# Performance work log

Measured on AMD Instinct MI355X. Metric: run time of the kernel, lower is better.

## Reference

```python
import jax, jax.numpy as jnp
import numpy as np

INPUT_DIM = 1024
HIDDEN_DIM = 1024

def setup_inputs() -> dict:
    key = jax.random.key(0)
    ks = jax.random.split(key, 9)
    s_in = 1.0 / np.sqrt(INPUT_DIM)
    s_h = 1.0 / np.sqrt(HIDDEN_DIM)
    x = jax.random.normal(ks[0], (4, 2048, INPUT_DIM), dtype=jnp.float32)
    Wq = jax.random.uniform(ks[1], (INPUT_DIM, HIDDEN_DIM), jnp.float32, -s_in, s_in)
    bq = jax.random.uniform(ks[2], (HIDDEN_DIM,), jnp.float32, -s_in, s_in)
    Wk = jax.random.uniform(ks[3], (INPUT_DIM, HIDDEN_DIM), jnp.float32, -s_in, s_in)
    bk = jax.random.uniform(ks[4], (HIDDEN_DIM,), jnp.float32, -s_in, s_in)
    Wv = jax.random.uniform(ks[5], (INPUT_DIM, HIDDEN_DIM), jnp.float32, -s_in, s_in)
    bv = jax.random.uniform(ks[6], (HIDDEN_DIM,), jnp.float32, -s_in, s_in)
    Wo = jax.random.uniform(ks[7], (HIDDEN_DIM, INPUT_DIM), jnp.float32, -s_h, s_h)
    bo = jax.random.uniform(ks[8], (INPUT_DIM,), jnp.float32, -s_h, s_h)
    return {"x": x, "Wq": Wq, "bq": bq, "Wk": Wk, "bk": bk, "Wv": Wv, "bv": bv, "Wo": Wo, "bo": bo}

def reference(x, Wq, bq, Wk, bk, Wv, bv, Wo, bo):
    # x: [B, S, D_in]; scale uses x.shape[-1] (faithful to source, which divides by sqrt(input_dim))
    scale = 1.0 / jnp.sqrt(jnp.asarray(x.shape[-1], dtype=x.dtype))
    Q = jnp.einsum('bsd,dh->bsh', x, Wq) + bq
    K = jnp.einsum('bsd,dh->bsh', x, Wk) + bk
    V = jnp.einsum('bsd,dh->bsh', x, Wv) + bv
    scores = jnp.einsum('bqh,bkh->bqk', Q, K) * scale  # [B, S, S]
    attn = jax.nn.softmax(scores, axis=-1)
    ctx = jnp.einsum('bqk,bkh->bqh', attn, V)
    return jnp.einsum('bsh,hd->bsd', ctx, Wo) + bo
```

## Files before the change

### kernel.cpp

```cpp
#include <hip/hip_runtime.h>

typedef __attribute__((ext_vector_type(8))) short bf16x8;
typedef __attribute__((ext_vector_type(4))) float f32x4;
typedef __attribute__((ext_vector_type(4))) unsigned short us4;

#define AS1 __attribute__((address_space(1)))
#define AS3 __attribute__((address_space(3)))

__device__ __forceinline__ unsigned short f2bf(float f) {
  unsigned u = __float_as_uint(f);
  u += 0x7fff + ((u >> 16) & 1);
  return (unsigned short)(u >> 16);
}

__device__ __forceinline__ void gload_lds16(const void* g, void* l) {
  __builtin_amdgcn_global_load_lds((const AS1 unsigned int*)g,
                                   (AS3 unsigned int*)l, 16, 0, 0);
}

#define MFMA16(a, b, c) __builtin_amdgcn_mfma_f32_16x16x32_bf16(a, b, c, 0, 0, 0)

template <typename OutT, bool BIAS, int MODE>
__global__ __launch_bounds__(512, 2) void gemm8p(
    const unsigned short* __restrict__ A,
    const unsigned short* __restrict__ Bt,
    OutT* __restrict__ C,
    unsigned short* __restrict__ Vt,
    const float* __restrict__ bias,
    int Kd, int lda, int ldb, int ldc,
    long sA, long sB, long sC,
    float scale) {
  constexpr int BOFF = 256 * 64;
  __shared__ unsigned short lds[2][512 * 64];

  const int bz = blockIdx.z;
  A  += (size_t)bz * sA + (size_t)blockIdx.x * 256 * lda;
  Bt += (size_t)bz * sB + (size_t)blockIdx.y * 256 * ldb;

  const int tid  = threadIdx.x;
  const int wave = tid >> 6;
  const int lane = tid & 63;
  const int wm   = wave >> 2;
  const int wn   = wave & 3;
  const int l15  = lane & 15;
  const int hi   = lane >> 4;
  const int sr  = (wave << 3) + (lane >> 3);
  const int sc8 = lane & 7;
  const int co0 = ((hi    ) ^ (lane & 7)) << 3;
  const int co1 = ((hi + 4) ^ (lane & 7)) << 3;
  const int rA0 = wm * 128 + l15;
  const int rB0 = wn * 32 + l15;

  auto stA = [&](int b, int k0, int r0) {
    const unsigned short* g =
        A + (size_t)(r0 + sr) * lda + (k0 + ((sc8 ^ (sr & 7)) << 3));
    gload_lds16(g, &lds[b][(r0 + (wave << 3)) * 64]);
  };
  auto stB = [&](int b, int k0, int r0) {
    const int lr = r0 + sr;
    const int gr = ((lr >> 5) & 3) * 64 + ((lr >> 7) << 5) + (lr & 31);
    const unsigned short* g =
        Bt + (size_t)gr * ldb + (k0 + ((sc8 ^ (lr & 7)) << 3));
    gload_lds16(g, &lds[b][BOFF + (r0 + (wave << 3)) * 64]);
  };

  f32x4 acc[8][4] = {};
  bf16x8 af[4][2], b0f[2][2], b1f[2][2];

  stA(0, 0, 0);   stA(0, 0, 128);
  stB(0, 0, 0);   stB(0, 0, 64);
  stB(0, 0, 128); stB(0, 0, 192);
  stA(0, 0, 64);  stA(0, 0, 192);
  asm volatile("s_waitcnt vmcnt(4)" ::: "memory");
  __builtin_amdgcn_s_barrier();

  const int NT = Kd >> 6;
  for (int t = 0; t < NT; ++t) {
    const int buf = t & 1;
    const int nb  = buf ^ 1;
    const int nk0 = (t + 1) << 6;
    const bool st = (t + 1) < NT;
    const unsigned short* Lr = &lds[buf][0];

#pragma unroll
    for (int mt = 0; mt < 4; ++mt) {
      af[mt][0] = *(const bf16x8*)&Lr[(rA0 + mt * 16) * 64 + co0];
      af[mt][1] = *(const bf16x8*)&Lr[(rA0 + mt * 16) * 64 + co1];
    }
#pragma unroll
    for (int n = 0; n < 2; ++n) {
      b0f[n][0] = *(const bf16x8*)&Lr[BOFF + (rB0 + n * 16) * 64 + co0];
      b0f[n][1] = *(const bf16x8*)&Lr[BOFF + (rB0 + n * 16) * 64 + co1];
    }
    if (st) { stA(nb, nk0, 0); stA(nb, nk0, 128); }
    __builtin_amdgcn_s_barrier();
    __builtin_amdgcn_s_setprio(1);
#pragma unroll
    for (int mt = 0; mt < 4; ++mt)
#pragma unroll
      for (int n = 0; n < 2; ++n) {
        acc[mt][n] = MFMA16(af[mt][0], b0f[n][0], acc[mt][n]);
        acc[mt][n] = MFMA16(af[mt][1], b0f[n][1], acc[mt][n]);
      }
    __builtin_amdgcn_s_setprio(0);
    asm volatile("s_waitcnt vmcnt(4)" ::: "memory");
    __builtin_amdgcn_s_barrier();

#pragma unroll
    for (int n = 0; n < 2; ++n) {
      b1f[n][0] = *(const bf16x8*)&Lr[BOFF + (128 + rB0 + n * 16) * 64 + co0];
      b1f[n][1] = *(const bf16x8*)&Lr[BOFF + (128 + rB0 + n * 16) * 64 + co1];
    }
    if (st) { stB(nb, nk0, 0); stB(nb, nk0, 64); }
    __builtin_amdgcn_s_barrier();
    __builtin_amdgcn_s_setprio(1);
#pragma unroll
    for (int mt = 0; mt < 4; ++mt)
#pragma unroll
      for (int n = 0; n < 2; ++n) {
        acc[mt][2 + n] = MFMA16(af[mt][0], b1f[n][0], acc[mt][2 + n]);
        acc[mt][2 + n] = MFMA16(af[mt][1], b1f[n][1], acc[mt][2 + n]);
      }
    __builtin_amdgcn_s_setprio(0);
    asm volatile("s_waitcnt vmcnt(4)" ::: "memory");
    __builtin_amdgcn_s_barrier();

#pragma unroll
    for (int mt = 0; mt < 4; ++mt) {
      af[mt][0] = *(const bf16x8*)&Lr[(64 + rA0 + mt * 16) * 64 + co0];
      af[mt][1] = *(const bf16x8*)&Lr[(64 + rA0 + mt * 16) * 64 + co1];
    }
    if (st) { stB(nb, nk0, 128); stB(nb, nk0, 192); }
    __builtin_amdgcn_s_barrier();
    __builtin_amdgcn_s_setprio(1);
#pragma unroll
    for (int mt = 0; mt < 4; ++mt)
#pragma unroll
      for (int n = 0; n < 2; ++n) {
        acc[4 + mt][2 + n] = MFMA16(af[mt][0], b1f[n][0], acc[4 + mt][2 + n]);
        acc[4 + mt][2 + n] = MFMA16(af[mt][1], b1f[n][1], acc[4 + mt][2 + n]);
      }
    __builtin_amdgcn_s_setprio(0);
    __builtin_amdgcn_s_barrier();

    if (st) { stA(nb, nk0, 64); stA(nb, nk0, 192); }
    __builtin_amdgcn_s_barrier();
    __builtin_amdgcn_s_setprio(1);
#pragma unroll
    for (int mt = 0; mt < 4; ++mt)
#pragma unroll
      for (int n = 0; n < 2; ++n) {
        acc[4 + mt][n] = MFMA16(af[mt][0], b0f[n][0], acc[4 + mt][n]);
        acc[4 + mt][n] = MFMA16(af[mt][1], b0f[n][1], acc[4 + mt][n]);
      }
    __builtin_amdgcn_s_setprio(0);
    asm volatile("s_waitcnt vmcnt(4)" ::: "memory");
    __builtin_amdgcn_s_barrier();
  }

  const int hi4  = hi << 2;
  const int row0 = blockIdx.x * 256 + wm * 128;
  const int col0 = blockIdx.y * 256 + wn * 64;

  if constexpr (MODE == 1) {
#pragma unroll
    for (int nt = 0; nt < 4; ++nt) {
      const int gcol  = col0 + nt * 16;
      const int piece = gcol >> 10;
      const float bv  = BIAS ? bias[gcol + l15] : 0.0f;
      if (piece < 2) {
        OutT* dst = C + (size_t)piece * sC;
        const int col = (gcol & 1023) + l15;
#pragma unroll
        for (int mt = 0; mt < 8; ++mt)
#pragma unroll
          for (int r = 0; r < 4; ++r) {
            const int row = row0 + mt * 16 + hi4 + r;
            dst[(size_t)row * ldc + col] = (OutT)f2bf(acc[mt][nt][r] * scale + bv);
          }
      } else {
        const int d = (gcol & 1023) + l15;
        const int b = blockIdx.x >> 3;
        const int sb = (blockIdx.x & 7) * 256 + wm * 128 + hi4;
#pragma unroll
        for (int mt = 0; mt < 8; ++mt) {
          us4 pk;
          pk.x = f2bf(acc[mt][nt][0] * scale + bv);
          pk.y = f2bf(acc[mt][nt][1] * scale + bv);
          pk.z = f2bf(acc[mt][nt][2] * scale + bv);
          pk.w = f2bf(acc[mt][nt][3] * scale + bv);
          *(us4*)&Vt[((size_t)b << 21) + (size_t)d * 2048 + sb + mt * 16] = pk;
        }
      }
    }
  } else {
    C += (size_t)bz * sC;
#pragma unroll
    for (int nt = 0; nt < 4; ++nt) {
      const int col = col0 + nt * 16 + l15;
      const float bv = BIAS ? bias[col] : 0.0f;
#pragma unroll
      for (int mt = 0; mt < 8; ++mt)
#pragma unroll
        for (int r = 0; r < 4; ++r) {
          const int row = row0 + mt * 16 + hi4 + r;
          const float v = acc[mt][nt][r] * scale + bv;
          if constexpr (sizeof(OutT) == 4)
            C[(size_t)row * ldc + col] = v;
          else
            C[(size_t)row * ldc + col] = (OutT)f2bf(v);
        }
    }
  }
}

__global__ void cvt_x(const float* __restrict__ in, unsigned short* __restrict__ out, int n4) {
  const int i = blockIdx.x * blockDim.x + threadIdx.x;
  if (i < n4) {
    const float4 v = ((const float4*)in)[i];
    uint2 o;
    o.x = (unsigned)f2bf(v.x) | ((unsigned)f2bf(v.y) << 16);
    o.y = (unsigned)f2bf(v.z) | ((unsigned)f2bf(v.w) << 16);
    ((uint2*)out)[i] = o;
  }
}

__global__ void cvtT_w4(const float* __restrict__ Wq, const float* __restrict__ Wk,
                        const float* __restrict__ Wv, const float* __restrict__ Wo,
                        unsigned short* __restrict__ Wqkvb, unsigned short* __restrict__ Wob) {
  __shared__ unsigned short tile[64][65];
  const int z = blockIdx.z;
  const float* in = (z == 0) ? Wq : (z == 1) ? Wk : (z == 2) ? Wv : Wo;
  unsigned short* out = (z == 3) ? Wob : Wqkvb + (size_t)z * 1024 * 1024;
  const int r0 = blockIdx.y * 64, c0 = blockIdx.x * 64;
  for (int i = threadIdx.y; i < 64; i += 4)
    tile[i][threadIdx.x] = f2bf(in[(size_t)(r0 + i) * 1024 + c0 + threadIdx.x]);
  __syncthreads();
  for (int i = threadIdx.y; i < 64; i += 4)
    out[(size_t)(c0 + i) * 1024 + r0 + threadIdx.x] = tile[threadIdx.x][i];
}

__global__ void concat_bias(const float* __restrict__ bq, const float* __restrict__ bk,
                            const float* __restrict__ bv, float* __restrict__ dst) {
  const int z = blockIdx.x;
  const float* src = (z == 0) ? bq : (z == 1) ? bk : bv;
  const int i = threadIdx.x;
  ((float4*)(dst + z * 1024))[i] = ((const float4*)src)[i];
}

__global__ __launch_bounds__(256) void softmax_bf16(unsigned short* __restrict__ scores) {
  unsigned short* p = scores + (size_t)blockIdx.x * 2048;
  const int t = threadIdx.x;
  uint4 raw = ((const uint4*)p)[t];
  float v[8];
  v[0] = __uint_as_float(raw.x << 16); v[1] = __uint_as_float(raw.x & 0xffff0000u);
  v[2] = __uint_as_float(raw.y << 16); v[3] = __uint_as_float(raw.y & 0xffff0000u);
  v[4] = __uint_as_float(raw.z << 16); v[5] = __uint_as_float(raw.z & 0xffff0000u);
  v[6] = __uint_as_float(raw.w << 16); v[7] = __uint_as_float(raw.w & 0xffff0000u);

  float m = v[0];
#pragma unroll
  for (int i = 1; i < 8; ++i) m = fmaxf(m, v[i]);
#pragma unroll
  for (int off = 32; off; off >>= 1) m = fmaxf(m, __shfl_xor(m, off, 64));

  __shared__ float red[4];
  __shared__ float bcast[2];
  const int wave = t >> 6, lane = t & 63;
  if (lane == 0) red[wave] = m;
  __syncthreads();
  if (t == 0) bcast[0] = fmaxf(fmaxf(red[0], red[1]), fmaxf(red[2], red[3]));
  __syncthreads();
  m = bcast[0];

  float s = 0.f;
#pragma unroll
  for (int i = 0; i < 8; ++i) { v[i] = __expf(v[i] - m); s += v[i]; }
#pragma unroll
  for (int off = 32; off; off >>= 1) s += __shfl_xor(s, off, 64);
  if (lane == 0) red[wave] = s;
  __syncthreads();
  if (t == 0) bcast[1] = red[0] + red[1] + red[2] + red[3];
  __syncthreads();
  const float inv = 1.0f / bcast[1];

  uint4 ov;
  ov.x = (unsigned)f2bf(v[0] * inv) | ((unsigned)f2bf(v[1] * inv) << 16);
  ov.y = (unsigned)f2bf(v[2] * inv) | ((unsigned)f2bf(v[3] * inv) << 16);
  ov.z = (unsigned)f2bf(v[4] * inv) | ((unsigned)f2bf(v[5] * inv) << 16);
  ov.w = (unsigned)f2bf(v[6] * inv) | ((unsigned)f2bf(v[7] * inv) << 16);
  ((uint4*)p)[t] = ov;
}

extern "C" void kernel_launch(void* const* d_in, const int* in_sizes, int n_in,
                              void* d_out, int out_size, void* d_ws, size_t ws_size,
                              hipStream_t stream) {
  const float* x  = (const float*)d_in[0];
  const float* Wq = (const float*)d_in[1];
  const float* bq = (const float*)d_in[2];
  const float* Wk = (const float*)d_in[3];
  const float* bk = (const float*)d_in[4];
  const float* Wv = (const float*)d_in[5];
  const float* bv = (const float*)d_in[6];
  const float* Wo = (const float*)d_in[7];
  const float* bo = (const float*)d_in[8];
  float* out = (float*)d_out;

  char* ws = (char*)d_ws;
  size_t off = 0;
  auto alloc = [&](size_t bytes) { char* p = ws + off; off += (bytes + 255) & ~255UL; return p; };
  unsigned short* xb    = (unsigned short*)alloc(8192UL * 1024 * 2);
  unsigned short* Wqkvb = (unsigned short*)alloc(3072UL * 1024 * 2);
  unsigned short* Wob   = (unsigned short*)alloc(1024UL * 1024 * 2);
  float*          bqkv  = (float*)alloc(3072UL * 4);
  unsigned short* Qb    = (unsigned short*)alloc(8192UL * 1024 * 2);
  unsigned short* Kb    = (unsigned short*)alloc(8192UL * 1024 * 2);
  unsigned short* Vtb   = (unsigned short*)alloc(4UL * 1024 * 2048 * 2);
  unsigned short* attn  = (unsigned short*)alloc(8192UL * 2048 * 2);
  unsigned short* ctxb  = (unsigned short*)alloc(8192UL * 1024 * 2);

  const dim3 blk(512);

  cvt_x<<<2097152 / 256, 256, 0, stream>>>(x, xb, 2097152);
  cvtT_w4<<<dim3(16, 16, 4), dim3(64, 4), 0, stream>>>(Wq, Wk, Wv, Wo, Wqkvb, Wob);
  concat_bias<<<3, 256, 0, stream>>>(bq, bk, bv, bqkv);

  gemm8p<unsigned short, true, 1><<<dim3(32, 12, 1), blk, 0, stream>>>(
      xb, Wqkvb, Qb, Vtb, bqkv, 1024, 1024, 1024, 1024, 0, 0, 8192L * 1024, 1.0f);

  gemm8p<unsigned short, false, 0><<<dim3(8, 8, 4), blk, 0, stream>>>(
      Qb, Kb, attn, nullptr, nullptr, 1024, 1024, 1024, 2048,
      2048L * 1024, 2048L * 1024, 2048L * 2048, 0.03125f);

  softmax_bf16<<<8192, 256, 0, stream>>>(attn);

  gemm8p<unsigned short, false, 0><<<dim3(8, 4, 4), blk, 0, stream>>>(
      attn, Vtb, ctxb, nullptr, nullptr, 2048, 2048, 2048, 1024,
      2048L * 2048, 1024L * 2048, 2048L * 1024, 1.0f);

  gemm8p<float, true, 0><<<dim3(32, 4, 1), blk, 0, stream>>>(
      ctxb, Wob, out, nullptr, bo, 1024, 1024, 1024, 1024, 0, 0, 0, 1.0f);
}
```

Before: 328.4 us.

## Issue next-tile global loads earlier and reorder epilogue stores by row

Moves all of the next K-tile's global-to-LDS loads into the first two phases of the main loop, so prefetch is issued earlier and the waitcnts are relaxed, letting memory latency overlap more MFMA work. The vmcnt wait on the last iteration becomes vmcnt(0). The epilogue is also restructured to hoist bias loads and to write all four column tiles for each row together, which gives better write locality. Issuing loads in a burst may raise contention, and the changed wait counts must still match the number of outstanding loads.

New measurement: 323.4 us. About the same (-1.5%).

```diff
diff --git a/kernel.cpp b/kernel.cpp
--- a/kernel.cpp
+++ b/kernel.cpp
@@ -92,7 +92,7 @@
       b0f[n][0] = *(const bf16x8*)&Lr[BOFF + (rB0 + n * 16) * 64 + co0];
       b0f[n][1] = *(const bf16x8*)&Lr[BOFF + (rB0 + n * 16) * 64 + co1];
     }
-    if (st) { stA(nb, nk0, 0); stA(nb, nk0, 128); }
+    if (st) { stA(nb, nk0, 0); stA(nb, nk0, 128); stB(nb, nk0, 0); stB(nb, nk0, 64); }
     __builtin_amdgcn_s_barrier();
     __builtin_amdgcn_s_setprio(1);
 #pragma unroll
@@ -103,7 +103,8 @@
         acc[mt][n] = MFMA16(af[mt][1], b0f[n][1], acc[mt][n]);
       }
     __builtin_amdgcn_s_setprio(0);
-    asm volatile("s_waitcnt vmcnt(4)" ::: "memory");
+    if (st) asm volatile("s_waitcnt vmcnt(4)" ::: "memory");
+    else    asm volatile("s_waitcnt vmcnt(0)" ::: "memory");
     __builtin_amdgcn_s_barrier();
 
 #pragma unroll
@@ -111,7 +112,7 @@
       b1f[n][0] = *(const bf16x8*)&Lr[BOFF + (128 + rB0 + n * 16) * 64 + co0];
       b1f[n][1] = *(const bf16x8*)&Lr[BOFF + (128 + rB0 + n * 16) * 64 + co1];
     }
-    if (st) { stB(nb, nk0, 0); stB(nb, nk0, 64); }
+    if (st) { stB(nb, nk0, 128); stB(nb, nk0, 192); stA(nb, nk0, 64); stA(nb, nk0, 192); }
     __builtin_amdgcn_s_barrier();
     __builtin_amdgcn_s_setprio(1);
 #pragma unroll
@@ -122,7 +123,6 @@
         acc[mt][2 + n] = MFMA16(af[mt][1], b1f[n][1], acc[mt][2 + n]);
       }
     __builtin_amdgcn_s_setprio(0);
-    asm volatile("s_waitcnt vmcnt(4)" ::: "memory");
     __builtin_amdgcn_s_barrier();
 
 #pragma unroll
@@ -130,7 +130,6 @@
       af[mt][0] = *(const bf16x8*)&Lr[(64 + rA0 + mt * 16) * 64 + co0];
       af[mt][1] = *(const bf16x8*)&Lr[(64 + rA0 + mt * 16) * 64 + co1];
     }
-    if (st) { stB(nb, nk0, 128); stB(nb, nk0, 192); }
     __builtin_amdgcn_s_barrier();
     __builtin_amdgcn_s_setprio(1);
 #pragma unroll
@@ -143,7 +142,6 @@
     __builtin_amdgcn_s_setprio(0);
     __builtin_amdgcn_s_barrier();
 
-    if (st) { stA(nb, nk0, 64); stA(nb, nk0, 192); }
     __builtin_amdgcn_s_barrier();
     __builtin_amdgcn_s_setprio(1);
 #pragma unroll
@@ -154,7 +152,7 @@
         acc[4 + mt][n] = MFMA16(af[mt][1], b0f[n][1], acc[4 + mt][n]);
       }
     __builtin_amdgcn_s_setprio(0);
-    asm volatile("s_waitcnt vmcnt(4)" ::: "memory");
+    if (st) asm volatile("s_waitcnt vmcnt(4)" ::: "memory");
     __builtin_amdgcn_s_barrier();
   }
 
@@ -163,54 +161,61 @@
   const int col0 = blockIdx.y * 256 + wn * 64;
 
   if constexpr (MODE == 1) {
-#pragma unroll
-    for (int nt = 0; nt < 4; ++nt) {
-      const int gcol  = col0 + nt * 16;
-      const int piece = gcol >> 10;
-      const float bv  = BIAS ? bias[gcol + l15] : 0.0f;
-      if (piece < 2) {
-        OutT* dst = C + (size_t)piece * sC;
-        const int col = (gcol & 1023) + l15;
-#pragma unroll
-        for (int mt = 0; mt < 8; ++mt)
-#pragma unroll
-          for (int r = 0; r < 4; ++r) {
-            const int row = row0 + mt * 16 + hi4 + r;
-            dst[(size_t)row * ldc + col] = (OutT)f2bf(acc[mt][nt][r] * scale + bv);
-          }
-      } else {
-        const int d = (gcol & 1023) + l15;
-        const int b = blockIdx.x >> 3;
-        const int sb = (blockIdx.x & 7) * 256 + wm * 128 + hi4;
+    const int piece = col0 >> 10;
+    float bvv[4];
+#pragma unroll
+    for (int nt = 0; nt < 4; ++nt)
+      bvv[nt] = BIAS ? bias[col0 + nt * 16 + l15] : 0.0f;
+    if (piece < 2) {
+      OutT* dst = C + (size_t)piece * sC;
+      const int cb = (col0 & 1023) + l15;
+#pragma unroll
+      for (int mt = 0; mt < 8; ++mt)
+#pragma unroll
+        for (int r = 0; r < 4; ++r) {
+          const size_t rowoff = (size_t)(row0 + mt * 16 + hi4 + r) * ldc;
+#pragma unroll
+          for (int nt = 0; nt < 4; ++nt)
+            dst[rowoff + cb + nt * 16] = (OutT)f2bf(acc[mt][nt][r] * scale + bvv[nt]);
+        }
+    } else {
+      const int b = blockIdx.x >> 3;
+      const int sb = (blockIdx.x & 7) * 256 + wm * 128 + hi4;
+#pragma unroll
+      for (int nt = 0; nt < 4; ++nt) {
+        const int d = ((col0 + nt * 16) & 1023) + l15;
 #pragma unroll
         for (int mt = 0; mt < 8; ++mt) {
           us4 pk;
-          pk.x = f2bf(acc[mt][nt][0] * scale + bv);
-          pk.y = f2bf(acc[mt][nt][1] * scale + bv);
-          pk.z = f2bf(acc[mt][nt][2] * scale + bv);
-          pk.w = f2bf(acc[mt][nt][3] * scale + bv);
+          pk.x = f2bf(acc[mt][nt][0] * scale + bvv[nt]);
+          pk.y = f2bf(acc[mt][nt][1] * scale + bvv[nt]);
+          pk.z = f2bf(acc[mt][nt][2] * scale + bvv[nt]);
+          pk.w = f2bf(acc[mt][nt][3] * scale + bvv[nt]);
           *(us4*)&Vt[((size_t)b << 21) + (size_t)d * 2048 + sb + mt * 16] = pk;
         }
       }
     }
   } else {
     C += (size_t)bz * sC;
-#pragma unroll
-    for (int nt = 0; nt < 4; ++nt) {
-      const int col = col0 + nt * 16 + l15;
-      const float bv = BIAS ? bias[col] : 0.0f;
-#pragma unroll
-      for (int mt = 0; mt < 8; ++mt)
-#pragma unroll
-        for (int r = 0; r < 4; ++r) {
-          const int row = row0 + mt * 16 + hi4 + r;
-          const float v = acc[mt][nt][r] * scale + bv;
+    float bvv[4];
+#pragma unroll
+    for (int nt = 0; nt < 4; ++nt)
+      bvv[nt] = BIAS ? bias[col0 + nt * 16 + l15] : 0.0f;
+    const int cb = col0 + l15;
+#pragma unroll
+    for (int mt = 0; mt < 8; ++mt)
+#pragma unroll
+      for (int r = 0; r < 4; ++r) {
+        const size_t rowoff = (size_t)(row0 + mt * 16 + hi4 + r) * ldc;
+#pragma unroll
+        for (int nt = 0; nt < 4; ++nt) {
+          const float v = acc[mt][nt][r] * scale + bvv[nt];
           if constexpr (sizeof(OutT) == 4)
-            C[(size_t)row * ldc + col] = v;
+            C[rowoff + cb + nt * 16] = v;
           else
-            C[(size_t)row * ldc + col] = (OutT)f2bf(v);
+            C[rowoff + cb + nt * 16] = (OutT)f2bf(v);
         }
-    }
+      }
   }
 }
 
```
